# Performance work log

Hardware: AMD Instinct MI355X
Metric: run time of the kernel (lower is better)

The kernel has to match this reference:

```python
import jax, jax.numpy as jnp
import numpy as np

N_NODES = 524288
N_EDGES = 786432
NUM_GRAPHS = 8192
NUM_NODE_TYPES = 16
NODE_DIM = 256
EDGE_DIM = 128
OUT_DIM = 1


def setup_inputs() -> dict:
    key = jax.random.key(0)
    ks = jax.random.split(key, 12)
    h_node = jax.random.uniform(ks[0], (N_NODES, NUM_NODE_TYPES), dtype=jnp.float32)
    pos_node = jax.random.normal(ks[1], (N_NODES, 3), dtype=jnp.float32)
    batch_node = jnp.sort(jax.random.randint(ks[2], (N_NODES,), 0, NUM_GRAPHS)).astype(jnp.int64)
    edge_index = jax.random.randint(ks[3], (2, N_EDGES), 0, N_NODES).astype(jnp.int64)
    batch_edge = jnp.sort(jax.random.randint(ks[4], (N_EDGES,), 0, NUM_GRAPHS)).astype(jnp.int64)
    s = 0.05
    W_node = jax.random.normal(ks[5], (NUM_NODE_TYPES, NODE_DIM), dtype=jnp.float32) * s
    W_edge = jax.random.normal(ks[6], (2 * NUM_NODE_TYPES, EDGE_DIM), dtype=jnp.float32) * s
    H = NODE_DIM + EDGE_DIM
    W1 = jax.random.normal(ks[7], (H, H), dtype=jnp.float32) * s
    b1 = jnp.zeros((H,), dtype=jnp.float32)
    W2 = jax.random.normal(ks[8], (H, OUT_DIM), dtype=jnp.float32) * s
    b2 = jnp.zeros((OUT_DIM,), dtype=jnp.float32)
    return {"h_node": h_node, "pos_node": pos_node, "batch_node": batch_node,
            "edge_index": edge_index, "batch_edge": batch_edge,
            "W_node": W_node, "W_edge": W_edge, "W1": W1, "b1": b1, "W2": W2, "b2": b2}


def _segment_mean(x, seg_ids, num_segments):
    # fused replacement for the original per-graph boolean-mask loop:
    # h[seg==k].mean(0) for all k, via one scatter-add + count normalize
    sums = jax.ops.segment_sum(x, seg_ids, num_segments=num_segments)
    cnts = jax.ops.segment_sum(jnp.ones((x.shape[0],), x.dtype), seg_ids, num_segments=num_segments)
    return sums / jnp.maximum(cnts, 1.0)[:, None]


def reference(h_node, pos_node, batch_node, edge_index, batch_edge,
              W_node, W_edge, W1, b1, W2, b2):
    # h_edge = cat(h_node[src], h_node[dst])  -> [E, 2*num_node_types]
    h_edge_raw = jnp.concatenate([h_node[edge_index[0]], h_node[edge_index[1]]], axis=-1)
    # num_timesteps == 0 path: plain embedders, no time embedding
    hn = h_node @ W_node          # [N, node_dim]
    he = h_edge_raw @ W_edge      # [E, edge_dim]
    # encoder treated as identity (NodeEdgeNet not in scope); pooling is the target op
    node_mean = _segment_mean(hn, batch_node, NUM_GRAPHS)  # [G, node_dim]
    edge_mean = _segment_mean(he, batch_edge, NUM_GRAPHS)  # [G, edge_dim]
    h_sub = jnp.concatenate([node_mean, edge_mean], axis=-1)  # [G, node_dim+edge_dim]
    # final MLP (num_layer=2): Linear -> ReLU -> Linear
    pred = jax.nn.relu(h_sub @ W1 + b1) @ W2 + b2  # [G, 1]
    return pred
```

## Files before the change

### kernel.cpp

```cpp
#include <hip/hip_runtime.h>

#define N_NODES_C   524288
#define N_EDGES_C   786432
#define NUM_GRAPHS_C 8192
#define NT 16
#define NODE_DIM_C 256
#define EDGE_DIM_C 128
#define HDIM 384
#define KC 48

#define FOLD_BLOCKS  72
#define EDGE_BLOCKS  16384
#define NODE_BLOCKS  2048
#define EDGE_BASE    FOLD_BLOCKS
#define NODE_BASE    (FOLD_BLOCKS + EDGE_BLOCKS)
#define TOTAL_BLOCKS (FOLD_BLOCKS + EDGE_BLOCKS + NODE_BLOCKS)
#define K0_BLOCKS    3072

#define WS_NM    0
#define WS_EM    524288
#define WS_WC    1572864
#define WS_ES    1646592
#define WS_NS    1679364

__device__ __forceinline__ void f4_add(float4& a, const float4 v) {
    a.x += v.x; a.y += v.y; a.z += v.z; a.w += v.w;
}

__device__ __forceinline__ void f4_shfl_xor_add(float4& a, int mask) {
    a.x += __shfl_xor(a.x, mask, 64);
    a.y += __shfl_xor(a.y, mask, 64);
    a.z += __shfl_xor(a.z, mask, 64);
    a.w += __shfl_xor(a.w, mask, 64);
}

__global__ __launch_bounds__(256) void k0_prep(
    const int* __restrict__ bnode, const int* __restrict__ bedge,
    int* __restrict__ estart, int* __restrict__ nstart, float* __restrict__ em) {
    int i = blockIdx.x * 256 + threadIdx.x;
    if (i < NUM_GRAPHS_C * 32) em[i] = 0.f;
    if (i < N_EDGES_C) {
        int g0 = bedge[i];
        int hi = (i + 1 < N_EDGES_C) ? bedge[i + 1] : NUM_GRAPHS_C;
        if (i == 0) for (int g = 0; g <= g0; ++g) estart[g] = 0;
        for (int g = g0 + 1; g <= hi; ++g) estart[g] = i + 1;
    }
    if (i < N_NODES_C) {
        int g0 = bnode[i];
        int hi = (i + 1 < N_NODES_C) ? bnode[i + 1] : NUM_GRAPHS_C;
        if (i == 0) for (int g = 0; g <= g0; ++g) nstart[g] = 0;
        for (int g = g0 + 1; g <= hi; ++g) nstart[g] = i + 1;
    }
}

__global__ __launch_bounds__(256) void km_mega(
    const float* __restrict__ h_node,
    const int* __restrict__ esrc, const int* __restrict__ edst,
    const int* __restrict__ estart, const int* __restrict__ nstart,
    const float* __restrict__ Wn, const float* __restrict__ We,
    const float* __restrict__ W1,
    float* __restrict__ nm, float* __restrict__ em, float* __restrict__ Wc) {
    int blk  = blockIdx.x;
    int wave = threadIdx.x >> 6;
    int lane = threadIdx.x & 63;
    const float4* h4 = (const float4*)h_node;
    const float4 z4 = make_float4(0.f, 0.f, 0.f, 0.f);

    if (blk < FOLD_BLOCKS) {
        int o = blk * 256 + threadIdx.x;
        if (o >= KC * HDIM) return;
        int k = o / HDIM, j = o % HDIM;
        float acc = 0.f;
        if (k < NT) {
            const float* wr = &Wn[k * NODE_DIM_C];
            #pragma unroll 16
            for (int kk = 0; kk < NODE_DIM_C; ++kk)
                acc = fmaf(wr[kk], W1[(size_t)kk * HDIM + j], acc);
        } else {
            const float* wr = &We[(k - NT) * EDGE_DIM_C];
            #pragma unroll 16
            for (int kk = 0; kk < EDGE_DIM_C; ++kk)
                acc = fmaf(wr[kk], W1[(size_t)(NODE_DIM_C + kk) * HDIM + j], acc);
        }
        Wc[o] = acc;
    } else if (blk < NODE_BASE) {
        int eb    = blk - EDGE_BASE;
        int slice = eb & 7;
        int g     = (eb >> 3) * 4 + wave;
        int s = estart[g], e = estart[g + 1];
        int eo   = lane >> 3;
        int p    = (lane >> 2) & 1;
        int quad = lane & 3;
        const int* __restrict__ idxp = p ? edst : esrc;
        float4 accA = z4, accB = z4;
        int iA = s + eo, iB = iA + 8;
        int nxA = (iA < e) ? idxp[iA] : -1;
        int nxB = (iB < e) ? idxp[iB] : -1;
        while (nxB >= 0) {
            int idxA = nxA, idxB = nxB;
            iA += 16; iB += 16;
            nxA = (iA < e) ? idxp[iA] : -1;
            nxB = (iB < e) ? idxp[iB] : -1;
            if ((idxA >> 16) == slice) f4_add(accA, h4[(size_t)idxA * 4 + quad]);
            if ((idxB >> 16) == slice) f4_add(accB, h4[(size_t)idxB * 4 + quad]);
        }
        if (nxA >= 0 && (nxA >> 16) == slice)
            f4_add(accA, h4[(size_t)nxA * 4 + quad]);
        f4_add(accA, accB);
        f4_shfl_xor_add(accA, 8);
        f4_shfl_xor_add(accA, 16);
        f4_shfl_xor_add(accA, 32);
        if (eo == 0) {
            float inv = 1.f / fmaxf((float)(e - s), 1.f);
            float* dst = &em[(size_t)g * 32 + p * 16 + quad * 4];
            atomicAdd(dst + 0, accA.x * inv);
            atomicAdd(dst + 1, accA.y * inv);
            atomicAdd(dst + 2, accA.z * inv);
            atomicAdd(dst + 3, accA.w * inv);
        }
    } else {
        int g = (blk - NODE_BASE) * 4 + wave;
        int s = nstart[g], e = nstart[g + 1];
        int row_off = lane >> 2;
        int quad    = lane & 3;
        float4 a0 = z4, a1 = z4;
        int i = s + row_off;
        for (; i + 16 < e; i += 32) {
            float4 v0 = h4[(size_t)i * 4 + quad];
            float4 v1 = h4[(size_t)(i + 16) * 4 + quad];
            f4_add(a0, v0);
            f4_add(a1, v1);
        }
        if (i < e) f4_add(a0, h4[(size_t)i * 4 + quad]);
        f4_add(a0, a1);
        f4_shfl_xor_add(a0, 4);
        f4_shfl_xor_add(a0, 8);
        f4_shfl_xor_add(a0, 16);
        f4_shfl_xor_add(a0, 32);
        if (row_off == 0) {
            float inv = 1.f / fmaxf((float)(e - s), 1.f);
            ((float4*)nm)[(size_t)g * 4 + quad] =
                make_float4(a0.x * inv, a0.y * inv, a0.z * inv, a0.w * inv);
        }
    }
}

#define GPB 16
__global__ __launch_bounds__(HDIM) void k3_mlp(
    const float* __restrict__ nm, const float* __restrict__ em,
    const float* __restrict__ Wc, const float* __restrict__ b1,
    const float* __restrict__ W2, const float* __restrict__ b2,
    float* __restrict__ pred) {
    int j = threadIdx.x;
    float wc[KC];
    #pragma unroll
    for (int k = 0; k < KC; ++k) wc[k] = Wc[k * HDIM + j];
    float b1j = b1[j], w2j = W2[j], b20 = b2[0];

    __shared__ float fs[GPB][KC];
    __shared__ float part[GPB][6];
    int g0 = blockIdx.x * GPB;
    #pragma unroll
    for (int t = j; t < GPB * KC; t += HDIM) {
        int g = t / KC, k = t % KC;
        fs[g][k] = (k < NT) ? nm[(size_t)(g0 + g) * NT + k]
                            : em[(size_t)(g0 + g) * 32 + (k - NT)];
    }
    __syncthreads();

    int wave = j >> 6, lane = j & 63;
    for (int g = 0; g < GPB; ++g) {
        float z = b1j;
        #pragma unroll
        for (int k = 0; k < KC; ++k) z = fmaf(fs[g][k], wc[k], z);
        z = fmaxf(z, 0.f);
        float p = z * w2j;
        #pragma unroll
        for (int off = 32; off > 0; off >>= 1) p += __shfl_down(p, off, 64);
        if (lane == 0) part[g][wave] = p;
    }
    __syncthreads();
    if (j < GPB) {
        float sacc = b20;
        #pragma unroll
        for (int w = 0; w < 6; ++w) sacc += part[j][w];
        pred[g0 + j] = sacc;
    }
}

extern "C" void kernel_launch(void* const* d_in, const int* in_sizes, int n_in,
                              void* d_out, int out_size, void* d_ws, size_t ws_size,
                              hipStream_t stream) {
    const float* h_node     = (const float*)d_in[0];
    const int*   batch_node = (const int*)d_in[2];
    const int*   edge_index = (const int*)d_in[3];
    const int*   batch_edge = (const int*)d_in[4];
    const float* W_node     = (const float*)d_in[5];
    const float* W_edge     = (const float*)d_in[6];
    const float* W1         = (const float*)d_in[7];
    const float* b1         = (const float*)d_in[8];
    const float* W2         = (const float*)d_in[9];
    const float* b2         = (const float*)d_in[10];
    float* pred = (float*)d_out;

    char* ws = (char*)d_ws;
    float* nm     = (float*)(ws + WS_NM);
    float* em     = (float*)(ws + WS_EM);
    float* Wc     = (float*)(ws + WS_WC);
    int*   estart = (int*)(ws + WS_ES);
    int*   nstart = (int*)(ws + WS_NS);

    const int* esrc = edge_index;
    const int* edst = edge_index + N_EDGES_C;

    k0_prep<<<K0_BLOCKS, 256, 0, stream>>>(batch_node, batch_edge, estart, nstart, em);
    km_mega<<<TOTAL_BLOCKS, 256, 0, stream>>>(
        h_node, esrc, edst, estart, nstart, W_node, W_edge, W1, nm, em, Wc);
    k3_mlp<<<NUM_GRAPHS_C / GPB, HDIM, 0, stream>>>(nm, em, Wc, b1, W2, b2, pred);
}
```

Before: 174.5 us.

## Bucket edge endpoints by node slice via counting sort before gather

Adds a counting-sort pass (count, two-level scan, scatter) that groups each edge endpoint index by (node slice, side, graph). The edge gather in the main kernel then reads only the indices in its own slice instead of scanning every edge of the graph and filtering, and it writes per-slice partial sums without atomics. The final MLP kernel sums the 8 slices and divides by the edge count. This adds four extra launches and atomic-heavy count and scatter passes over all edges in exchange for less redundant index reading in the gather.

```diff
diff --git a/kernel.cpp b/kernel.cpp
--- a/kernel.cpp
+++ b/kernel.cpp
@@ -9,19 +9,24 @@
 #define HDIM 384
 #define KC 48
 
-#define FOLD_BLOCKS  72
-#define EDGE_BLOCKS  16384
-#define NODE_BLOCKS  2048
-#define EDGE_BASE    FOLD_BLOCKS
-#define NODE_BASE    (FOLD_BLOCKS + EDGE_BLOCKS)
-#define TOTAL_BLOCKS (FOLD_BLOCKS + EDGE_BLOCKS + NODE_BLOCKS)
-#define K0_BLOCKS    3072
+#define NBIN        131072
+#define FOLD_BLOCKS 72
+#define NODE_BLOCKS 2048
+#define EDGE_BLOCKS 16384
+#define NODE_BASE   FOLD_BLOCKS
+#define EDGE_BASE   (FOLD_BLOCKS + NODE_BLOCKS)
+#define TOTAL_BLOCKS (FOLD_BLOCKS + NODE_BLOCKS + EDGE_BLOCKS)
 
 #define WS_NM    0
-#define WS_EM    524288
-#define WS_WC    1572864
-#define WS_ES    1646592
-#define WS_NS    1679364
+#define WS_EM8   524288
+#define WS_WC    8912896
+#define WS_ES    8986624
+#define WS_NS    9019456
+#define WS_CNT   9052288
+#define WS_OFFL  9576576
+#define WS_BSUM  10100864
+#define WS_BPRE  10101376
+#define WS_REC   10101888
 
 __device__ __forceinline__ void f4_add(float4& a, const float4 v) {
     a.x += v.x; a.y += v.y; a.z += v.z; a.w += v.w;
@@ -34,32 +39,93 @@
     a.w += __shfl_xor(a.w, mask, 64);
 }
 
-__global__ __launch_bounds__(256) void k0_prep(
+__global__ __launch_bounds__(256) void kz_zero(int* __restrict__ cnt) {
+    ((int4*)cnt)[blockIdx.x * 256 + threadIdx.x] = make_int4(0, 0, 0, 0);
+}
+
+__global__ __launch_bounds__(256) void ka_count(
     const int* __restrict__ bnode, const int* __restrict__ bedge,
-    int* __restrict__ estart, int* __restrict__ nstart, float* __restrict__ em) {
+    const int* __restrict__ esrc, const int* __restrict__ edst,
+    int* __restrict__ cnt, int* __restrict__ estart, int* __restrict__ nstart) {
     int i = blockIdx.x * 256 + threadIdx.x;
-    if (i < NUM_GRAPHS_C * 32) em[i] = 0.f;
     if (i < N_EDGES_C) {
-        int g0 = bedge[i];
+        int g  = bedge[i];
         int hi = (i + 1 < N_EDGES_C) ? bedge[i + 1] : NUM_GRAPHS_C;
-        if (i == 0) for (int g = 0; g <= g0; ++g) estart[g] = 0;
-        for (int g = g0 + 1; g <= hi; ++g) estart[g] = i + 1;
+        if (i == 0) for (int q = 0; q <= g; ++q) estart[q] = 0;
+        for (int q = g + 1; q <= hi; ++q) estart[q] = i + 1;
+        int a = esrc[i], b = edst[i];
+        atomicAdd(&cnt[(((a >> 16) * 2 + 0) << 13) + g], 1);
+        atomicAdd(&cnt[(((b >> 16) * 2 + 1) << 13) + g], 1);
     }
     if (i < N_NODES_C) {
-        int g0 = bnode[i];
+        int g  = bnode[i];
         int hi = (i + 1 < N_NODES_C) ? bnode[i + 1] : NUM_GRAPHS_C;
-        if (i == 0) for (int g = 0; g <= g0; ++g) nstart[g] = 0;
-        for (int g = g0 + 1; g <= hi; ++g) nstart[g] = i + 1;
-    }
+        if (i == 0) for (int q = 0; q <= g; ++q) nstart[q] = 0;
+        for (int q = g + 1; q <= hi; ++q) nstart[q] = i + 1;
+    }
+}
+
+__global__ __launch_bounds__(256) void kb_scan1(
+    const int* __restrict__ cnt, int* __restrict__ offl, int* __restrict__ bsum) {
+    __shared__ int sh[256];
+    int b = blockIdx.x, t = threadIdx.x;
+    int4 v = ((const int4*)(cnt + b * 1024))[t];
+    int tsum = v.x + v.y + v.z + v.w;
+    sh[t] = tsum;
+    __syncthreads();
+    for (int d = 1; d < 256; d <<= 1) {
+        int add = (t >= d) ? sh[t - d] : 0;
+        __syncthreads();
+        sh[t] += add;
+        __syncthreads();
+    }
+    int base = (t == 0) ? 0 : sh[t - 1];
+    int4 o;
+    o.x = base; o.y = base + v.x; o.z = base + v.x + v.y; o.w = base + v.x + v.y + v.z;
+    ((int4*)(offl + b * 1024))[t] = o;
+    if (t == 255) bsum[b] = sh[255];
+}
+
+__global__ __launch_bounds__(128) void kc_scan2(
+    const int* __restrict__ bsum, int* __restrict__ bpre) {
+    __shared__ int sh[128];
+    int t = threadIdx.x;
+    sh[t] = bsum[t];
+    __syncthreads();
+    for (int d = 1; d < 128; d <<= 1) {
+        int add = (t >= d) ? sh[t - d] : 0;
+        __syncthreads();
+        sh[t] += add;
+        __syncthreads();
+    }
+    bpre[t] = (t == 0) ? 0 : sh[t - 1];
+}
+
+__global__ __launch_bounds__(256) void ks_scatter(
+    const int* __restrict__ bedge,
+    const int* __restrict__ esrc, const int* __restrict__ edst,
+    int* __restrict__ cnt, const int* __restrict__ offl,
+    const int* __restrict__ bpre, int* __restrict__ rec) {
+    int i = blockIdx.x * 256 + threadIdx.x;
+    if (i >= N_EDGES_C) return;
+    int g = bedge[i];
+    int a = esrc[i], b = edst[i];
+    int binA = (((a >> 16) * 2 + 0) << 13) + g;
+    int binB = (((b >> 16) * 2 + 1) << 13) + g;
+    int pA = atomicSub(&cnt[binA], 1) - 1;
+    rec[offl[binA] + bpre[binA >> 10] + pA] = a;
+    int pB = atomicSub(&cnt[binB], 1) - 1;
+    rec[offl[binB] + bpre[binB >> 10] + pB] = b;
 }
 
 __global__ __launch_bounds__(256) void km_mega(
     const float* __restrict__ h_node,
-    const int* __restrict__ esrc, const int* __restrict__ edst,
     const int* __restrict__ estart, const int* __restrict__ nstart,
+    const int* __restrict__ offl, const int* __restrict__ bpre,
+    const int* __restrict__ rec,
     const float* __restrict__ Wn, const float* __restrict__ We,
     const float* __restrict__ W1,
-    float* __restrict__ nm, float* __restrict__ em, float* __restrict__ Wc) {
+    float* __restrict__ nm, float* __restrict__ em8, float* __restrict__ Wc) {
     int blk  = blockIdx.x;
     int wave = threadIdx.x >> 6;
     int lane = threadIdx.x & 63;
@@ -83,43 +149,10 @@
                 acc = fmaf(wr[kk], W1[(size_t)(NODE_DIM_C + kk) * HDIM + j], acc);
         }
         Wc[o] = acc;
-    } else if (blk < NODE_BASE) {
-        int eb    = blk - EDGE_BASE;
-        int slice = eb & 7;
-        int g     = (eb >> 3) * 4 + wave;
-        int s = estart[g], e = estart[g + 1];
-        int eo   = lane >> 3;
-        int p    = (lane >> 2) & 1;
-        int quad = lane & 3;
-        const int* __restrict__ idxp = p ? edst : esrc;
-        float4 accA = z4, accB = z4;
-        int iA = s + eo, iB = iA + 8;
-        int nxA = (iA < e) ? idxp[iA] : -1;
-        int nxB = (iB < e) ? idxp[iB] : -1;
-        while (nxB >= 0) {
-            int idxA = nxA, idxB = nxB;
-            iA += 16; iB += 16;
-            nxA = (iA < e) ? idxp[iA] : -1;
-            nxB = (iB < e) ? idxp[iB] : -1;
-            if ((idxA >> 16) == slice) f4_add(accA, h4[(size_t)idxA * 4 + quad]);
-            if ((idxB >> 16) == slice) f4_add(accB, h4[(size_t)idxB * 4 + quad]);
-        }
-        if (nxA >= 0 && (nxA >> 16) == slice)
-            f4_add(accA, h4[(size_t)nxA * 4 + quad]);
-        f4_add(accA, accB);
-        f4_shfl_xor_add(accA, 8);
-        f4_shfl_xor_add(accA, 16);
-        f4_shfl_xor_add(accA, 32);
-        if (eo == 0) {
-            float inv = 1.f / fmaxf((float)(e - s), 1.f);
-            float* dst = &em[(size_t)g * 32 + p * 16 + quad * 4];
-            atomicAdd(dst + 0, accA.x * inv);
-            atomicAdd(dst + 1, accA.y * inv);
-            atomicAdd(dst + 2, accA.z * inv);
-            atomicAdd(dst + 3, accA.w * inv);
-        }
-    } else {
-        int g = (blk - NODE_BASE) * 4 + wave;
+    } else if (blk < EDGE_BASE) {
+        int r = blk - NODE_BASE;
+        int s8 = r & 7;
+        int g  = s8 * 1024 + (r >> 3) * 4 + wave;
         int s = nstart[g], e = nstart[g + 1];
         int row_off = lane >> 2;
         int quad    = lane & 3;
@@ -142,12 +175,47 @@
             ((float4*)nm)[(size_t)g * 4 + quad] =
                 make_float4(a0.x * inv, a0.y * inv, a0.z * inv, a0.w * inv);
         }
+    } else {
+        int r     = blk - EDGE_BASE;
+        int slice = r & 7;
+        int g     = (r >> 3) * 4 + wave;
+        int binS  = ((slice * 2 + 0) << 13) + g;
+        int binD  = binS + (1 << 13);
+        int stS = offl[binS] + bpre[binS >> 10];
+        int enS = offl[binS + 1] + bpre[(binS + 1) >> 10];
+        int stD = offl[binD] + bpre[binD >> 10];
+        int enD = (binD == NBIN - 1) ? 2 * N_EDGES_C
+                                     : offl[binD + 1] + bpre[(binD + 1) >> 10];
+        int slot = lane >> 3;
+        int p    = (lane >> 2) & 1;
+        int quad = lane & 3;
+        int st = p ? stD : stS;
+        int en = p ? enD : enS;
+        int cmax = max(enS - stS, enD - stD);
+        int T = (cmax + 7) >> 3;
+        float4 acc = z4;
+        int i = st + slot;
+        int idx = (i < en) ? rec[i] : -1;
+        for (int t = 1; t < T; ++t) {
+            int i2 = i + 8;
+            int nx = (i2 < en) ? rec[i2] : -1;
+            if (idx >= 0) f4_add(acc, h4[(size_t)idx * 4 + quad]);
+            idx = nx; i = i2;
+        }
+        if (idx >= 0) f4_add(acc, h4[(size_t)idx * 4 + quad]);
+        f4_shfl_xor_add(acc, 8);
+        f4_shfl_xor_add(acc, 16);
+        f4_shfl_xor_add(acc, 32);
+        if (slot == 0) {
+            ((float4*)em8)[((size_t)(slice * NUM_GRAPHS_C + g)) * 8 + p * 4 + quad] = acc;
+        }
     }
 }
 
 #define GPB 16
 __global__ __launch_bounds__(HDIM) void k3_mlp(
-    const float* __restrict__ nm, const float* __restrict__ em,
+    const float* __restrict__ nm, const float* __restrict__ em8,
+    const int* __restrict__ estart,
     const float* __restrict__ Wc, const float* __restrict__ b1,
     const float* __restrict__ W2, const float* __restrict__ b2,
     float* __restrict__ pred) {
@@ -160,11 +228,21 @@
     __shared__ float fs[GPB][KC];
     __shared__ float part[GPB][6];
     int g0 = blockIdx.x * GPB;
-    #pragma unroll
     for (int t = j; t < GPB * KC; t += HDIM) {
         int g = t / KC, k = t % KC;
-        fs[g][k] = (k < NT) ? nm[(size_t)(g0 + g) * NT + k]
-                            : em[(size_t)(g0 + g) * 32 + (k - NT)];
+        int G = g0 + g;
+        float val;
+        if (k < NT) {
+            val = nm[(size_t)G * NT + k];
+        } else {
+            float ssum = 0.f;
+            #pragma unroll
+            for (int s = 0; s < 8; ++s)
+                ssum += em8[((size_t)(s * NUM_GRAPHS_C + G)) * 32 + (k - NT)];
+            float ec = (float)(estart[G + 1] - estart[G]);
+            val = ssum / fmaxf(ec, 1.f);
+        }
+        fs[g][k] = val;
     }
     __syncthreads();
 
@@ -205,16 +283,27 @@
 
     char* ws = (char*)d_ws;
     float* nm     = (float*)(ws + WS_NM);
-    float* em     = (float*)(ws + WS_EM);
+    float* em8    = (float*)(ws + WS_EM8);
     float* Wc     = (float*)(ws + WS_WC);
     int*   estart = (int*)(ws + WS_ES);
     int*   nstart = (int*)(ws + WS_NS);
+    int*   cnt    = (int*)(ws + WS_CNT);
+    int*   offl   = (int*)(ws + WS_OFFL);
+    int*   bsum   = (int*)(ws + WS_BSUM);
+    int*   bpre   = (int*)(ws + WS_BPRE);
+    int*   rec    = (int*)(ws + WS_REC);
 
     const int* esrc = edge_index;
     const int* edst = edge_index + N_EDGES_C;
 
-    k0_prep<<<K0_BLOCKS, 256, 0, stream>>>(batch_node, batch_edge, estart, nstart, em);
-    km_mega<<<TOTAL_BLOCKS, 256, 0, stream>>>(
-        h_node, esrc, edst, estart, nstart, W_node, W_edge, W1, nm, em, Wc);
-    k3_mlp<<<NUM_GRAPHS_C / GPB, HDIM, 0, stream>>>(nm, em, Wc, b1, W2, b2, pred);
-}
+    kz_zero  <<<128,  256, 0, stream>>>(cnt);
+    ka_count <<<3072, 256, 0, stream>>>(batch_node, batch_edge, esrc, edst,
+                                        cnt, estart, nstart);
+    kb_scan1 <<<128,  256, 0, stream>>>(cnt, offl, bsum);
+    kc_scan2 <<<1,    128, 0, stream>>>(bsum, bpre);
+    ks_scatter<<<3072,256, 0, stream>>>(batch_edge, esrc, edst, cnt, offl, bpre, rec);
+    km_mega  <<<TOTAL_BLOCKS, 256, 0, stream>>>(
+        h_node, estart, nstart, offl, bpre, rec, W_node, W_edge, W1, nm, em8, Wc);
+    k3_mlp   <<<NUM_GRAPHS_C / GPB, HDIM, 0, stream>>>(
+        nm, em8, estart, Wc, b1, W2, b2, pred);
+}
```

After: 387.0 us. +121.9%, slower.
